# Performance work log

Measured on AMD Instinct MI355X. Metric: run time of the kernel, lower is better.

The kernel has to match this reference:

```python
import jax, jax.numpy as jnp
import numpy as np

# (npoint, radius, nsample) per SA stage, from module defaults
SA_CFG = [(2048, 0.2, 64), (1024, 0.4, 32), (512, 0.6, 16), (256, 1.2, 8)]


def fps(xyz, npoint):
    """Farthest point sampling, CUDA-kernel semantics: start at index 0.
    xyz: [B,N,3] -> idx [B,npoint] int32."""
    B, N, _ = xyz.shape

    def step(carry, _):
        dist, far = carry
        centroid = jnp.take_along_axis(xyz, far[:, None, None], axis=1)  # [B,1,3]
        d = jnp.sum((xyz - centroid) ** 2, axis=-1)                      # [B,N]
        dist = jnp.minimum(dist, d)
        return (dist, jnp.argmax(dist, axis=-1).astype(jnp.int32)), far

    init = (jnp.full((B, N), 1e10, xyz.dtype), jnp.zeros((B,), jnp.int32))
    _, idxs = jax.lax.scan(step, init, None, length=npoint)  # [npoint,B]
    return idxs.T


def gather(pts, idx):
    """pts: [B,N,C], idx: [B,...] int -> [B,...,C]."""
    return jax.vmap(lambda p, i: p[i])(pts, idx)


def ball_query(xyz, new_xyz, radius, nsample):
    """First-nsample-in-ball semantics of pointnet2 ball_query; pads with the
    first found neighbor. xyz:[B,N,3], new_xyz:[B,S,3] -> [B,S,nsample] int."""
    N = xyz.shape[1]
    # squared dists via ||a||^2 + ||b||^2 - 2ab to avoid a [B,S,N,3] temp
    d2 = (jnp.sum(new_xyz ** 2, -1)[:, :, None]
          + jnp.sum(xyz ** 2, -1)[:, None, :]
          - 2.0 * jnp.einsum('bsc,bnc->bsn', new_xyz, xyz))
    cand = jnp.where(d2 < radius * radius, jnp.arange(N)[None, None, :], N)
    idx = jnp.sort(cand, axis=-1)[..., :nsample]
    first = idx[..., :1]  # center itself is always in the ball (d2==0)
    return jnp.where(idx == N, first, idx)


def sa_stage(xyz, feats, npoint, radius, nsample, layers):
    """One PointnetSAModuleVotes: FPS + ball query + normalized relative xyz
    (use_xyz=True, normalize_xyz=True) + shared MLP + max pool over nsample."""
    fidx = fps(xyz, npoint)
    new_xyz = gather(xyz, fidx)                         # [B,S,3]
    nidx = ball_query(xyz, new_xyz, radius, nsample)    # [B,S,K]
    rel = (gather(xyz, nidx) - new_xyz[:, :, None, :]) / radius  # [B,S,K,3]
    x = rel if feats is None else jnp.concatenate([rel, gather(feats, nidx)], -1)
    for w, b in layers:  # shared 1x1-conv MLP (BN folded), ReLU
        x = jax.nn.relu(x @ w + b)
    return new_xyz, jnp.max(x, axis=2)                  # [B,S,C_out]


def setup_inputs() -> dict:
    key = jax.random.key(0)
    ks = jax.random.split(key, 16)
    inp = {"pointcloud": jax.random.normal(ks[0], (4, 16384, 3), jnp.float32)}
    dims = [(3, 64, 64, 128), (131, 128, 128, 256),
            (259, 256, 256, 512), (515, 512, 512, 512)]
    k = 1
    for s, d in enumerate(dims, 1):
        for l in range(3):
            inp[f"w{s}{l}"] = jax.random.normal(
                jax.random.fold_in(ks[k], l), (d[l], d[l + 1]), jnp.float32) * 0.02
            inp[f"b{s}{l}"] = jnp.zeros((d[l + 1],), jnp.float32)
        k += 1
    return inp


def reference(pointcloud,
              w10, b10, w11, b11, w12, b12,
              w20, b20, w21, b21, w22, b22,
              w30, b30, w31, b31, w32, b32,
              w40, b40, w41, b41, w42, b42):
    stage_params = [
        [(w10, b10), (w11, b11), (w12, b12)],
        [(w20, b20), (w21, b21), (w22, b22)],
        [(w30, b30), (w31, b31), (w32, b32)],
        [(w40, b40), (w41, b41), (w42, b42)],
    ]
    xyz = pointcloud[..., :3]
    feats = None  # input_feature_dim == 0
    for (npoint, radius, nsample), layers in zip(SA_CFG, stage_params):
        xyz, feats = sa_stage(xyz, feats, npoint, radius, nsample, layers)
    return xyz, feats  # sa4_xyz [B,256,3], sa4_features [B,256,512]
```

## Files before the change

### kernel.cpp

```cpp
#include <hip/hip_runtime.h>
#include <hip/hip_bf16.h>


#define B_SZ 4

typedef float v2f __attribute__((ext_vector_type(2)));
typedef unsigned long long u64;

__device__ __forceinline__ v2f pk_add(v2f a, v2f b) {
  v2f d;
  asm("v_pk_add_f32 %0, %1, %2" : "=v"(d) : "v"(a), "v"(b));
  return d;
}
__device__ __forceinline__ v2f pk_mul(v2f a, v2f b) {
  v2f d;
  asm("v_pk_mul_f32 %0, %1, %2" : "=v"(d) : "v"(a), "v"(b));
  return d;
}

template <int CTRL>
__device__ __forceinline__ u64 dpp_u64(u64 v) {
  int lo = (int)(unsigned)v;
  int hi = (int)(unsigned)(v >> 32);
  int nlo = __builtin_amdgcn_update_dpp(lo, lo, CTRL, 0xF, 0xF, false);
  int nhi = __builtin_amdgcn_update_dpp(hi, hi, CTRL, 0xF, 0xF, false);
  return ((u64)(unsigned)nhi << 32) | (unsigned)nlo;
}

__device__ __forceinline__ u64 wave_max_u64(u64 P) {
  u64 o;
  o = dpp_u64<0x111>(P); P = o > P ? o : P;
  o = dpp_u64<0x112>(P); P = o > P ? o : P;
  o = dpp_u64<0x114>(P); P = o > P ? o : P;
  o = dpp_u64<0x118>(P); P = o > P ? o : P;
  o = dpp_u64<0x142>(P); P = o > P ? o : P;
  o = dpp_u64<0x143>(P); P = o > P ? o : P;
  return P;
}

template <int N, int NPOINT, int T, bool XYZ_IN_LDS>
__global__ __launch_bounds__(T, (T / 256 > 0) ? T / 256 : 1) void fps_kernel(
    const float* __restrict__ xyz, int* __restrict__ fidx) {
#pragma clang fp contract(off)
  constexpr int PT = N / T;
  static_assert(PT % 2 == 0, "PT even");
  constexpr int NP2 = PT / 2;
  constexpr int NW = T / 64;
  constexpr int NACC = (NP2 >= 4) ? 4 : NP2;
  constexpr int LN = XYZ_IN_LDS ? N : 1;
  const int b = blockIdx.x;
  const int t = threadIdx.x;
  const int lane = t & 63;
  const int wv = t >> 6;
  const float* base = xyz + (size_t)b * N * 3;

  v2f px[NP2], py[NP2], pz[NP2], dv[NP2];
  __shared__ __align__(16) u64 s_pack[2][NW];
  __shared__ float s_x[LN], s_y[LN], s_z[LN];

#pragma unroll
  for (int j = 0; j < NP2; ++j) {
    int i0 = t + (2 * j) * T;
    int i1 = t + (2 * j + 1) * T;
    px[j][0] = base[i0 * 3 + 0]; py[j][0] = base[i0 * 3 + 1];
    pz[j][0] = base[i0 * 3 + 2];
    px[j][1] = base[i1 * 3 + 0]; py[j][1] = base[i1 * 3 + 1];
    pz[j][1] = base[i1 * 3 + 2];
    dv[j][0] = 1e10f; dv[j][1] = 1e10f;
    if constexpr (XYZ_IN_LDS) {
      s_x[i0] = px[j][0]; s_y[i0] = py[j][0]; s_z[i0] = pz[j][0];
      s_x[i1] = px[j][1]; s_y[i1] = py[j][1]; s_z[i1] = pz[j][1];
    }
  }
  __syncthreads();

  int far = 0;
  int p = 0;
  for (int it = 0; it < NPOINT; ++it) {
    if (t == 0) fidx[b * NPOINT + it] = far;
    float cx, cy, cz;
    if constexpr (XYZ_IN_LDS) {
      cx = s_x[far]; cy = s_y[far]; cz = s_z[far];
    } else {
      cx = base[far * 3 + 0]; cy = base[far * 3 + 1]; cz = base[far * 3 + 2];
    }
    const float nx = -cx, ny = -cy, nz = -cz;
    const v2f c2x = {nx, nx}, c2y = {ny, ny}, c2z = {nz, nz};

    float mx[NACC];
#pragma unroll
    for (int q = 0; q < NACC; ++q) mx[q] = -1.0f;

#pragma unroll
    for (int j = 0; j < NP2; ++j) {
      v2f dx = pk_add(px[j], c2x);
      v2f dy = pk_add(py[j], c2y);
      v2f dz = pk_add(pz[j], c2z);
      v2f xx = pk_mul(dx, dx);
      v2f yy = pk_mul(dy, dy);
      v2f zz = pk_mul(dz, dz);
      v2f s = pk_add(xx, yy);
      v2f d = pk_add(s, zz);
      float nd0 = fminf(dv[j][0], d[0]);
      float nd1 = fminf(dv[j][1], d[1]);
      dv[j][0] = nd0; dv[j][1] = nd1;
      const int q = j % NACC;
      mx[q] = fmaxf(fmaxf(nd0, nd1), mx[q]);
    }
    float m = mx[0];
#pragma unroll
    for (int q = 1; q < NACC; ++q) m = fmaxf(m, mx[q]);

    int bk = 0;
#pragma unroll
    for (int j = NP2 - 1; j >= 0; --j) {
      if (dv[j][1] == m) bk = 2 * j + 1;
      if (dv[j][0] == m) bk = 2 * j;
    }

    int idx = t + bk * T;
    u64 P = ((u64)__float_as_uint(m) << 32) | (unsigned)(N - idx);
    P = wave_max_u64(P);
    if (lane == 63) s_pack[p][wv] = P;
    __syncthreads();
    u64 bbp = s_pack[p][0];
#pragma unroll
    for (int w = 1; w < NW; ++w) {
      u64 v = s_pack[p][w];
      bbp = v > bbp ? v : bbp;
    }
    far = N - (int)(unsigned)(bbp & 0xffffffffull);
    p ^= 1;
  }
}

__global__ void gather_xyz_kernel(const float* __restrict__ xyz,
                                  const int* __restrict__ fidx,
                                  float* __restrict__ out, int N, int S) {
  int s = blockIdx.x * blockDim.x + threadIdx.x;
  int b = blockIdx.y;
  if (s < S) {
    int i = fidx[b * S + s];
    out[((size_t)(b * S + s)) * 3 + 0] = xyz[((size_t)(b * N + i)) * 3 + 0];
    out[((size_t)(b * S + s)) * 3 + 1] = xyz[((size_t)(b * N + i)) * 3 + 1];
    out[((size_t)(b * S + s)) * 3 + 2] = xyz[((size_t)(b * N + i)) * 3 + 2];
  }
}

template <int N, int NS>
__global__ __launch_bounds__(256) void ball_query_kernel(
    const float* __restrict__ xyz, const float* __restrict__ new_xyz,
    int* __restrict__ nidx, int S, float r2) {
#pragma clang fp contract(off)
  const int wv = threadIdx.x >> 6;
  const int lane = threadIdx.x & 63;
  const int b = blockIdx.y;
  const int s = blockIdx.x * 4 + wv;
  __shared__ int s_idx[4][NS];
  const float* base = xyz + (size_t)b * N * 3;

  float cx = new_xyz[((size_t)(b * S + s)) * 3 + 0];
  float cy = new_xyz[((size_t)(b * S + s)) * 3 + 1];
  float cz = new_xyz[((size_t)(b * S + s)) * 3 + 2];
  float sc = (cx * cx + cy * cy) + cz * cz;

  int found = 0;
  for (int i0 = 0; i0 < N && found < NS; i0 += 64) {
    int i = i0 + lane;
    float x = base[i * 3 + 0];
    float y = base[i * 3 + 1];
    float z = base[i * 3 + 2];
    float sx = (x * x + y * y) + z * z;
    float dt = (cx * x + cy * y) + cz * z;
    float d2 = (sc + sx) - 2.0f * dt;
    bool inb = d2 < r2;
    unsigned long long m = __ballot(inb);
    if (inb) {
      int pos = found + __popcll(m & ((1ull << lane) - 1));
      if (pos < NS) s_idx[wv][pos] = i;
    }
    found += __popcll(m);
  }
  __syncthreads();
  int fcnt = found < NS ? found : NS;
  int first = s_idx[wv][0];
  int* outp = nidx + ((size_t)(b * S + s)) * NS;
  for (int j = lane; j < NS; j += 64) outp[j] = (j < fcnt) ? s_idx[wv][j] : first;
}

template <int R, int RG, int CG, int CMAXP, int CIN, int COUT>
__device__ __forceinline__ void mlp_layer(float* act, const float* __restrict__ w,
                                          const float* __restrict__ bias, int tid) {
  constexpr int RPT = R / RG;
  constexpr int CPT = COUT / CG;
  static_assert(RG * CG == 256, "thread grid");
  const int rg = tid / CG;
  const int cg = tid % CG;

  float acc[RPT][CPT];
#pragma unroll
  for (int rr = 0; rr < RPT; ++rr)
#pragma unroll
    for (int cc = 0; cc < CPT; ++cc) acc[rr][cc] = 0.f;

  constexpr int K4 = (CIN / 4) * 4;
  for (int k = 0; k < K4; k += 4) {
    float4 a[RPT];
#pragma unroll
    for (int rr = 0; rr < RPT; ++rr)
      a[rr] = *(const float4*)(&act[(rg * RPT + rr) * CMAXP + k]);
    float wvv[4][CPT];
#pragma unroll
    for (int kk = 0; kk < 4; ++kk)
#pragma unroll
      for (int cc = 0; cc < CPT; ++cc)
        wvv[kk][cc] = w[(size_t)(k + kk) * COUT + cg + cc * CG];
#pragma unroll
    for (int rr = 0; rr < RPT; ++rr) {
      float4 av = a[rr];
#pragma unroll
      for (int cc = 0; cc < CPT; ++cc) {
        acc[rr][cc] += av.x * wvv[0][cc];
        acc[rr][cc] += av.y * wvv[1][cc];
        acc[rr][cc] += av.z * wvv[2][cc];
        acc[rr][cc] += av.w * wvv[3][cc];
      }
    }
  }
#pragma unroll 1
  for (int k = K4; k < CIN; ++k) {
    float wvv[CPT];
#pragma unroll
    for (int cc = 0; cc < CPT; ++cc) wvv[cc] = w[(size_t)k * COUT + cg + cc * CG];
#pragma unroll
    for (int rr = 0; rr < RPT; ++rr) {
      float av = act[(rg * RPT + rr) * CMAXP + k];
#pragma unroll
      for (int cc = 0; cc < CPT; ++cc) acc[rr][cc] += av * wvv[cc];
    }
  }
  __syncthreads();
#pragma unroll
  for (int rr = 0; rr < RPT; ++rr)
#pragma unroll
    for (int cc = 0; cc < CPT; ++cc) {
      int co = cg + cc * CG;
      float v = acc[rr][cc] + bias[co];
      act[(rg * RPT + rr) * CMAXP + co] = fmaxf(v, 0.f);
    }
  __syncthreads();
}

template <int NS, int G, int CPREV, int CO0, int CO1, int CO2, int RG, int CG, int CMAXP>
__global__ __launch_bounds__(256) void group_mlp_kernel(
    const float* __restrict__ xyz, const float* __restrict__ new_xyz,
    const float* __restrict__ feats, const int* __restrict__ nidx,
    const float* __restrict__ w0, const float* __restrict__ b0,
    const float* __restrict__ w1, const float* __restrict__ b1,
    const float* __restrict__ w2, const float* __restrict__ b2,
    float* __restrict__ out, int N, int S, float radius) {
  constexpr int R = NS * G;
  constexpr int CIN = 3 + CPREV;
  __shared__ __align__(16) float act[R * CMAXP];
  const int tid = threadIdx.x;
  const int b = blockIdx.y;
  const int s0 = blockIdx.x * G;

  for (int i = tid; i < R * CIN; i += 256) {
    int row = i / CIN;
    int ch = i - row * CIN;
    int g = row / NS;
    int j = row - g * NS;
    int sidx = s0 + g;
    int n = nidx[((size_t)(b * S + sidx)) * NS + j];
    float v;
    if constexpr (CPREV == 0) {
      v = (xyz[((size_t)(b * N + n)) * 3 + ch] -
           new_xyz[((size_t)(b * S + sidx)) * 3 + ch]) /
          radius;
    } else {
      if (ch < 3) {
        v = (xyz[((size_t)(b * N + n)) * 3 + ch] -
             new_xyz[((size_t)(b * S + sidx)) * 3 + ch]) /
            radius;
      } else {
        v = feats[((size_t)(b * N + n)) * CPREV + (ch - 3)];
      }
    }
    act[row * CMAXP + ch] = v;
  }
  __syncthreads();

  mlp_layer<R, RG, CG, CMAXP, CIN, CO0>(act, w0, b0, tid);
  mlp_layer<R, RG, CG, CMAXP, CO0, CO1>(act, w1, b1, tid);
  mlp_layer<R, RG, CG, CMAXP, CO1, CO2>(act, w2, b2, tid);

  for (int i = tid; i < G * CO2; i += 256) {
    int g = i / CO2;
    int co = i - g * CO2;
    float m = act[(g * NS) * CMAXP + co];
    for (int j = 1; j < NS; ++j) m = fmaxf(m, act[(g * NS + j) * CMAXP + co]);
    out[((size_t)(b * S + s0 + g)) * CO2 + co] = m;
  }
}

extern "C" void kernel_launch(void* const* d_in, const int* in_sizes, int n_in,
                              void* d_out, int out_size, void* d_ws, size_t ws_size,
                              hipStream_t stream) {
  (void)in_sizes; (void)n_in; (void)out_size; (void)ws_size;
  const float* pc = (const float*)d_in[0];
  const float* W[4][3];
  const float* Bb[4][3];
  for (int s = 0; s < 4; ++s)
    for (int l = 0; l < 3; ++l) {
      W[s][l] = (const float*)d_in[1 + s * 6 + l * 2];
      Bb[s][l] = (const float*)d_in[2 + s * 6 + l * 2];
    }

  char* wsp = (char*)d_ws;
  int* fidx = (int*)wsp;
  int* nidx = (int*)(wsp + (32 << 10));
  float* xyzA = (float*)(wsp + (32 << 10) + (2 << 20));
  float* xyzB = xyzA + B_SZ * 2048 * 3;
  float* featA = xyzB + B_SZ * 2048 * 3;
  float* featB = featA + B_SZ * 2048 * 128;
  float* oxyz = (float*)d_out;
  float* ofeat = oxyz + B_SZ * 256 * 3;

  hipLaunchKernelGGL((fps_kernel<16384, 2048, 512, false>), dim3(B_SZ), dim3(512), 0, stream,
                     pc, fidx);
  hipLaunchKernelGGL(gather_xyz_kernel, dim3(32, B_SZ), dim3(64), 0, stream,
                     pc, fidx, xyzA, 16384, 2048);
  hipLaunchKernelGGL((ball_query_kernel<16384, 64>), dim3(512, B_SZ), dim3(256), 0, stream,
                     pc, xyzA, nidx, 2048, (float)(0.2 * 0.2));
  hipLaunchKernelGGL((group_mlp_kernel<64, 1, 0, 64, 64, 128, 8, 32, 128>),
                     dim3(2048, B_SZ), dim3(256), 0, stream,
                     pc, xyzA, (const float*)nullptr, nidx,
                     W[0][0], Bb[0][0], W[0][1], Bb[0][1], W[0][2], Bb[0][2],
                     featA, 16384, 2048, 0.2f);

  hipLaunchKernelGGL((fps_kernel<2048, 1024, 512, true>), dim3(B_SZ), dim3(512), 0, stream,
                     xyzA, fidx);
  hipLaunchKernelGGL(gather_xyz_kernel, dim3(16, B_SZ), dim3(64), 0, stream,
                     xyzA, fidx, xyzB, 2048, 1024);
  hipLaunchKernelGGL((ball_query_kernel<2048, 32>), dim3(256, B_SZ), dim3(256), 0, stream,
                     xyzA, xyzB, nidx, 1024, (float)(0.4 * 0.4));
  hipLaunchKernelGGL((group_mlp_kernel<32, 1, 128, 128, 128, 256, 4, 64, 256>),
                     dim3(1024, B_SZ), dim3(256), 0, stream,
                     xyzA, xyzB, featA, nidx,
                     W[1][0], Bb[1][0], W[1][1], Bb[1][1], W[1][2], Bb[1][2],
                     featB, 2048, 1024, 0.4f);

  hipLaunchKernelGGL((fps_kernel<1024, 512, 256, true>), dim3(B_SZ), dim3(256), 0, stream,
                     xyzB, fidx);
  hipLaunchKernelGGL(gather_xyz_kernel, dim3(8, B_SZ), dim3(64), 0, stream,
                     xyzB, fidx, xyzA, 1024, 512);
  hipLaunchKernelGGL((ball_query_kernel<1024, 16>), dim3(128, B_SZ), dim3(256), 0, stream,
                     xyzB, xyzA, nidx, 512, (float)(0.6 * 0.6));
  hipLaunchKernelGGL((group_mlp_kernel<16, 1, 256, 256, 256, 512, 2, 128, 512>),
                     dim3(512, B_SZ), dim3(256), 0, stream,
                     xyzB, xyzA, featB, nidx,
                     W[2][0], Bb[2][0], W[2][1], Bb[2][1], W[2][2], Bb[2][2],
                     featA, 1024, 512, 0.6f);

  hipLaunchKernelGGL((fps_kernel<512, 256, 256, true>), dim3(B_SZ), dim3(256), 0, stream,
                     xyzA, fidx);
  hipLaunchKernelGGL(gather_xyz_kernel, dim3(4, B_SZ), dim3(64), 0, stream,
                     xyzA, fidx, oxyz, 512, 256);
  hipLaunchKernelGGL((ball_query_kernel<512, 8>), dim3(64, B_SZ), dim3(256), 0, stream,
                     xyzA, oxyz, nidx, 256, (float)(1.2 * 1.2));
  hipLaunchKernelGGL((group_mlp_kernel<8, 2, 512, 512, 512, 512, 2, 128, 516>),
                     dim3(128, B_SZ), dim3(256), 0, stream,
                     xyzA, oxyz, featA, nidx,
                     W[3][0], Bb[3][0], W[3][1], Bb[3][1], W[3][2], Bb[3][2],
                     ofeat, 512, 256, 1.2f);
}
```

Before: 5.181 ms.

## Fuse next-stage FPS into group MLP kernel and broadcast centroid via LDS

The FPS for stage k+1 depends only on stage k's sampled xyz, not on its features. It is now run inside the same launch as stage k's group MLP: the first B blocks run FPS at raised priority, and the rest run the MLP, so the serial FPS overlaps the MLP work. Stage-1 FPS no longer reads the centroid from global memory after the block reduction. Each wave fetches its local winner's coordinates before the barrier and shares them through LDS. The change also adds occupancy hints to the MLP kernels and moves the fused FPS to 256 threads. Risks include LDS sizing that is the maximum of both uses, and fewer threads for the stage-2 FPS.

```diff
diff --git a/kernel.cpp b/kernel.cpp
--- a/kernel.cpp
+++ b/kernel.cpp
@@ -38,16 +38,15 @@
   return P;
 }
 
-template <int N, int NPOINT, int T, bool XYZ_IN_LDS>
-__global__ __launch_bounds__(T, (T / 256 > 0) ? T / 256 : 1) void fps_kernel(
-    const float* __restrict__ xyz, int* __restrict__ fidx) {
+template <int N, int NPOINT, int T>
+__global__ __launch_bounds__(T, 2) void fps1_kernel(const float* __restrict__ xyz,
+                                                    int* __restrict__ fidx) {
 #pragma clang fp contract(off)
   constexpr int PT = N / T;
   static_assert(PT % 2 == 0, "PT even");
   constexpr int NP2 = PT / 2;
   constexpr int NW = T / 64;
   constexpr int NACC = (NP2 >= 4) ? 4 : NP2;
-  constexpr int LN = XYZ_IN_LDS ? N : 1;
   const int b = blockIdx.x;
   const int t = threadIdx.x;
   const int lane = t & 63;
@@ -55,8 +54,8 @@
   const float* base = xyz + (size_t)b * N * 3;
 
   v2f px[NP2], py[NP2], pz[NP2], dv[NP2];
-  __shared__ __align__(16) u64 s_pack[2][NW];
-  __shared__ float s_x[LN], s_y[LN], s_z[LN];
+  __shared__ __align__(16) u64 s_key[2][NW];
+  __shared__ float s_cx[2][NW], s_cy[2][NW], s_cz[2][NW];
 
 #pragma unroll
   for (int j = 0; j < NP2; ++j) {
@@ -67,24 +66,14 @@
     px[j][1] = base[i1 * 3 + 0]; py[j][1] = base[i1 * 3 + 1];
     pz[j][1] = base[i1 * 3 + 2];
     dv[j][0] = 1e10f; dv[j][1] = 1e10f;
-    if constexpr (XYZ_IN_LDS) {
-      s_x[i0] = px[j][0]; s_y[i0] = py[j][0]; s_z[i0] = pz[j][0];
-      s_x[i1] = px[j][1]; s_y[i1] = py[j][1]; s_z[i1] = pz[j][1];
-    }
-  }
-  __syncthreads();
+  }
 
   int far = 0;
+  float cenx = base[0], ceny = base[1], cenz = base[2];
   int p = 0;
   for (int it = 0; it < NPOINT; ++it) {
     if (t == 0) fidx[b * NPOINT + it] = far;
-    float cx, cy, cz;
-    if constexpr (XYZ_IN_LDS) {
-      cx = s_x[far]; cy = s_y[far]; cz = s_z[far];
-    } else {
-      cx = base[far * 3 + 0]; cy = base[far * 3 + 1]; cz = base[far * 3 + 2];
-    }
-    const float nx = -cx, ny = -cy, nz = -cz;
+    const float nx = -cenx, ny = -ceny, nz = -cenz;
     const v2f c2x = {nx, nx}, c2y = {ny, ny}, c2z = {nz, nz};
 
     float mx[NACC];
@@ -121,12 +110,109 @@
     int idx = t + bk * T;
     u64 P = ((u64)__float_as_uint(m) << 32) | (unsigned)(N - idx);
     P = wave_max_u64(P);
-    if (lane == 63) s_pack[p][wv] = P;
+
+    int wf = N - __builtin_amdgcn_readlane((int)(unsigned)(P & 0xffffffffull), 63);
+    float wx = base[wf * 3 + 0];
+    float wy = base[wf * 3 + 1];
+    float wz = base[wf * 3 + 2];
+    if (lane == 63) s_key[p][wv] = P;
+    if (lane == 0) { s_cx[p][wv] = wx; s_cy[p][wv] = wy; s_cz[p][wv] = wz; }
     __syncthreads();
-    u64 bbp = s_pack[p][0];
+    u64 bb = s_key[p][0];
+    int mw = 0;
 #pragma unroll
     for (int w = 1; w < NW; ++w) {
-      u64 v = s_pack[p][w];
+      u64 v = s_key[p][w];
+      if (v > bb) { bb = v; mw = w; }
+    }
+    far = N - (int)(unsigned)(bb & 0xffffffffull);
+    cenx = s_cx[p][mw]; ceny = s_cy[p][mw]; cenz = s_cz[p][mw];
+    p ^= 1;
+  }
+}
+
+template <int N, int NPOINT, int T>
+__device__ __forceinline__ void fps_body_lds(char* smem,
+                                             const float* __restrict__ xyz,
+                                             int* __restrict__ fidx, int b) {
+#pragma clang fp contract(off)
+  constexpr int PT = N / T;
+  static_assert(PT % 2 == 0, "PT even");
+  constexpr int NP2 = PT / 2;
+  constexpr int NW = T / 64;
+  constexpr int NACC = (NP2 >= 4) ? 4 : NP2;
+  u64* s_pack = (u64*)smem;
+  float* s_x = (float*)(smem + 2 * NW * sizeof(u64));
+  float* s_y = s_x + N;
+  float* s_z = s_y + N;
+  const int t = threadIdx.x;
+  const int lane = t & 63;
+  const int wv = t >> 6;
+  const float* base = xyz + (size_t)b * N * 3;
+
+  v2f px[NP2], py[NP2], pz[NP2], dv[NP2];
+#pragma unroll
+  for (int j = 0; j < NP2; ++j) {
+    int i0 = t + (2 * j) * T;
+    int i1 = t + (2 * j + 1) * T;
+    px[j][0] = base[i0 * 3 + 0]; py[j][0] = base[i0 * 3 + 1];
+    pz[j][0] = base[i0 * 3 + 2];
+    px[j][1] = base[i1 * 3 + 0]; py[j][1] = base[i1 * 3 + 1];
+    pz[j][1] = base[i1 * 3 + 2];
+    dv[j][0] = 1e10f; dv[j][1] = 1e10f;
+    s_x[i0] = px[j][0]; s_y[i0] = py[j][0]; s_z[i0] = pz[j][0];
+    s_x[i1] = px[j][1]; s_y[i1] = py[j][1]; s_z[i1] = pz[j][1];
+  }
+  __syncthreads();
+
+  int far = 0;
+  int p = 0;
+  for (int it = 0; it < NPOINT; ++it) {
+    if (t == 0) fidx[b * NPOINT + it] = far;
+    float cx = s_x[far], cy = s_y[far], cz = s_z[far];
+    const float nx = -cx, ny = -cy, nz = -cz;
+    const v2f c2x = {nx, nx}, c2y = {ny, ny}, c2z = {nz, nz};
+
+    float mx[NACC];
+#pragma unroll
+    for (int q = 0; q < NACC; ++q) mx[q] = -1.0f;
+
+#pragma unroll
+    for (int j = 0; j < NP2; ++j) {
+      v2f dx = pk_add(px[j], c2x);
+      v2f dy = pk_add(py[j], c2y);
+      v2f dz = pk_add(pz[j], c2z);
+      v2f xx = pk_mul(dx, dx);
+      v2f yy = pk_mul(dy, dy);
+      v2f zz = pk_mul(dz, dz);
+      v2f s = pk_add(xx, yy);
+      v2f d = pk_add(s, zz);
+      float nd0 = fminf(dv[j][0], d[0]);
+      float nd1 = fminf(dv[j][1], d[1]);
+      dv[j][0] = nd0; dv[j][1] = nd1;
+      const int q = j % NACC;
+      mx[q] = fmaxf(fmaxf(nd0, nd1), mx[q]);
+    }
+    float m = mx[0];
+#pragma unroll
+    for (int q = 1; q < NACC; ++q) m = fmaxf(m, mx[q]);
+
+    int bk = 0;
+#pragma unroll
+    for (int j = NP2 - 1; j >= 0; --j) {
+      if (dv[j][1] == m) bk = 2 * j + 1;
+      if (dv[j][0] == m) bk = 2 * j;
+    }
+
+    int idx = t + bk * T;
+    u64 P = ((u64)__float_as_uint(m) << 32) | (unsigned)(N - idx);
+    P = wave_max_u64(P);
+    if (lane == 63) s_pack[p * NW + wv] = P;
+    __syncthreads();
+    u64 bbp = s_pack[p * NW + 0];
+#pragma unroll
+    for (int w = 1; w < NW; ++w) {
+      u64 v = s_pack[p * NW + w];
       bbp = v > bbp ? v : bbp;
     }
     far = N - (int)(unsigned)(bbp & 0xffffffffull);
@@ -252,19 +338,18 @@
 }
 
 template <int NS, int G, int CPREV, int CO0, int CO1, int CO2, int RG, int CG, int CMAXP>
-__global__ __launch_bounds__(256) void group_mlp_kernel(
-    const float* __restrict__ xyz, const float* __restrict__ new_xyz,
+__device__ __forceinline__ void group_mlp_body(
+    char* smem, const float* __restrict__ xyz, const float* __restrict__ new_xyz,
     const float* __restrict__ feats, const int* __restrict__ nidx,
     const float* __restrict__ w0, const float* __restrict__ b0,
     const float* __restrict__ w1, const float* __restrict__ b1,
     const float* __restrict__ w2, const float* __restrict__ b2,
-    float* __restrict__ out, int N, int S, float radius) {
+    float* __restrict__ out, int N, int S, float radius, int sblk, int b) {
   constexpr int R = NS * G;
   constexpr int CIN = 3 + CPREV;
-  __shared__ __align__(16) float act[R * CMAXP];
+  float* act = (float*)smem;
   const int tid = threadIdx.x;
-  const int b = blockIdx.y;
-  const int s0 = blockIdx.x * G;
+  const int s0 = sblk * G;
 
   for (int i = tid; i < R * CIN; i += 256) {
     int row = i / CIN;
@@ -304,6 +389,46 @@
   }
 }
 
+template <int NS, int G, int CPREV, int CO0, int CO1, int CO2, int RG, int CG, int CMAXP>
+__global__ __launch_bounds__(256, 4) void group_mlp_kernel(
+    const float* __restrict__ xyz, const float* __restrict__ new_xyz,
+    const float* __restrict__ feats, const int* __restrict__ nidx,
+    const float* __restrict__ w0, const float* __restrict__ b0,
+    const float* __restrict__ w1, const float* __restrict__ b1,
+    const float* __restrict__ w2, const float* __restrict__ b2,
+    float* __restrict__ out, int N, int S, float radius) {
+  __shared__ __align__(16) char smem[NS * G * CMAXP * 4];
+  group_mlp_body<NS, G, CPREV, CO0, CO1, CO2, RG, CG, CMAXP>(
+      smem, xyz, new_xyz, feats, nidx, w0, b0, w1, b1, w2, b2, out, N, S,
+      radius, blockIdx.x, blockIdx.y);
+}
+
+template <int FN, int FNP, int FT, int NS, int G, int CPREV, int CO0, int CO1,
+          int CO2, int RG, int CG, int CMAXP>
+__global__ __launch_bounds__(256, 4) void fused_fps_mlp_kernel(
+    const float* __restrict__ fpts, int* __restrict__ fidx,
+    const float* __restrict__ xyz, const float* __restrict__ new_xyz,
+    const float* __restrict__ feats, const int* __restrict__ nidx,
+    const float* __restrict__ w0, const float* __restrict__ b0,
+    const float* __restrict__ w1, const float* __restrict__ b1,
+    const float* __restrict__ w2, const float* __restrict__ b2,
+    float* __restrict__ out, int N, int S, float radius, int SBLK) {
+  constexpr int FPS_B = 2 * (FT / 64) * (int)sizeof(u64) + 3 * FN * 4;
+  constexpr int MLP_B = NS * G * CMAXP * 4;
+  constexpr int SB = (FPS_B > MLP_B) ? FPS_B : MLP_B;
+  __shared__ __align__(16) char smem[SB];
+  if ((int)blockIdx.x < B_SZ) {
+    __builtin_amdgcn_s_setprio(1);
+    fps_body_lds<FN, FNP, FT>(smem, fpts, fidx, blockIdx.x);
+    __builtin_amdgcn_s_setprio(0);
+  } else {
+    int bid = (int)blockIdx.x - B_SZ;
+    group_mlp_body<NS, G, CPREV, CO0, CO1, CO2, RG, CG, CMAXP>(
+        smem, xyz, new_xyz, feats, nidx, w0, b0, w1, b1, w2, b2, out, N, S,
+        radius, bid % SBLK, bid / SBLK);
+  }
+}
+
 extern "C" void kernel_launch(void* const* d_in, const int* in_sizes, int n_in,
                               void* d_out, int out_size, void* d_ws, size_t ws_size,
                               hipStream_t stream) {
@@ -327,48 +452,49 @@
   float* oxyz = (float*)d_out;
   float* ofeat = oxyz + B_SZ * 256 * 3;
 
-  hipLaunchKernelGGL((fps_kernel<16384, 2048, 512, false>), dim3(B_SZ), dim3(512), 0, stream,
+  hipLaunchKernelGGL((fps1_kernel<16384, 2048, 512>), dim3(B_SZ), dim3(512), 0, stream,
                      pc, fidx);
   hipLaunchKernelGGL(gather_xyz_kernel, dim3(32, B_SZ), dim3(64), 0, stream,
                      pc, fidx, xyzA, 16384, 2048);
   hipLaunchKernelGGL((ball_query_kernel<16384, 64>), dim3(512, B_SZ), dim3(256), 0, stream,
                      pc, xyzA, nidx, 2048, (float)(0.2 * 0.2));
-  hipLaunchKernelGGL((group_mlp_kernel<64, 1, 0, 64, 64, 128, 8, 32, 128>),
-                     dim3(2048, B_SZ), dim3(256), 0, stream,
+
+  hipLaunchKernelGGL((fused_fps_mlp_kernel<2048, 1024, 256,
+                                           64, 1, 0, 64, 64, 128, 8, 32, 128>),
+                     dim3(B_SZ + 2048 * B_SZ), dim3(256), 0, stream,
+                     xyzA, fidx,
                      pc, xyzA, (const float*)nullptr, nidx,
                      W[0][0], Bb[0][0], W[0][1], Bb[0][1], W[0][2], Bb[0][2],
-                     featA, 16384, 2048, 0.2f);
-
-  hipLaunchKernelGGL((fps_kernel<2048, 1024, 512, true>), dim3(B_SZ), dim3(512), 0, stream,
-                     xyzA, fidx);
+                     featA, 16384, 2048, 0.2f, 2048);
   hipLaunchKernelGGL(gather_xyz_kernel, dim3(16, B_SZ), dim3(64), 0, stream,
                      xyzA, fidx, xyzB, 2048, 1024);
   hipLaunchKernelGGL((ball_query_kernel<2048, 32>), dim3(256, B_SZ), dim3(256), 0, stream,
                      xyzA, xyzB, nidx, 1024, (float)(0.4 * 0.4));
-  hipLaunchKernelGGL((group_mlp_kernel<32, 1, 128, 128, 128, 256, 4, 64, 256>),
-                     dim3(1024, B_SZ), dim3(256), 0, stream,
+
+  hipLaunchKernelGGL((fused_fps_mlp_kernel<1024, 512, 256,
+                                           32, 1, 128, 128, 128, 256, 4, 64, 256>),
+                     dim3(B_SZ + 1024 * B_SZ), dim3(256), 0, stream,
+                     xyzB, fidx,
                      xyzA, xyzB, featA, nidx,
                      W[1][0], Bb[1][0], W[1][1], Bb[1][1], W[1][2], Bb[1][2],
-                     featB, 2048, 1024, 0.4f);
-
-  hipLaunchKernelGGL((fps_kernel<1024, 512, 256, true>), dim3(B_SZ), dim3(256), 0, stream,
-                     xyzB, fidx);
+                     featB, 2048, 1024, 0.4f, 1024);
   hipLaunchKernelGGL(gather_xyz_kernel, dim3(8, B_SZ), dim3(64), 0, stream,
                      xyzB, fidx, xyzA, 1024, 512);
   hipLaunchKernelGGL((ball_query_kernel<1024, 16>), dim3(128, B_SZ), dim3(256), 0, stream,
                      xyzB, xyzA, nidx, 512, (float)(0.6 * 0.6));
-  hipLaunchKernelGGL((group_mlp_kernel<16, 1, 256, 256, 256, 512, 2, 128, 512>),
-                     dim3(512, B_SZ), dim3(256), 0, stream,
+
+  hipLaunchKernelGGL((fused_fps_mlp_kernel<512, 256, 256,
+                                           16, 1, 256, 256, 256, 512, 2, 128, 512>),
+                     dim3(B_SZ + 512 * B_SZ), dim3(256), 0, stream,
+                     xyzA, fidx,
                      xyzB, xyzA, featB, nidx,
                      W[2][0], Bb[2][0], W[2][1], Bb[2][1], W[2][2], Bb[2][2],
-                     featA, 1024, 512, 0.6f);
-
-  hipLaunchKernelGGL((fps_kernel<512, 256, 256, true>), dim3(B_SZ), dim3(256), 0, stream,
-                     xyzA, fidx);
+                     featA, 1024, 512, 0.6f, 512);
   hipLaunchKernelGGL(gather_xyz_kernel, dim3(4, B_SZ), dim3(64), 0, stream,
                      xyzA, fidx, oxyz, 512, 256);
   hipLaunchKernelGGL((ball_query_kernel<512, 8>), dim3(64, B_SZ), dim3(256), 0, stream,
                      xyzA, oxyz, nidx, 256, (float)(1.2 * 1.2));
+
   hipLaunchKernelGGL((group_mlp_kernel<8, 2, 512, 512, 512, 512, 2, 128, 516>),
                      dim3(128, B_SZ), dim3(256), 0, stream,
                      xyzA, oxyz, featA, nidx,
```

New measurement: 5.031 ms. -2.9%, faster.
